# Optimization experiments

Measured on AMD Instinct MI355X. Metric: run time of the kernel, lower is better.

## Reference

```python
import jax, jax.numpy as jnp
import numpy as np

STATE_BITS = 10          # L: bits of trellis state
SHIFT_BITS = 2           # K: bits shifted in per step -> 2^K predecessors
CHUNK = 4                # chunk_size: values emitted per trellis step
S = 1 << STATE_BITS      # number of states (codebook rows)
NPRED = 1 << SHIFT_BITS  # predecessors per state
HI = 1 << (STATE_BITS - SHIFT_BITS)


def setup_inputs() -> dict:
    key = jax.random.key(0)
    k1, k2 = jax.random.split(key)
    array = jax.random.normal(k1, (1024, 1024), dtype=jnp.float32)
    codebook = jax.random.normal(k2, (S, CHUNK), dtype=jnp.float32)
    return {"array": array, "codebook": codebook, "block_size": 16}


def _viterbi(x, codebook):
    # x: [T, CHUNK, B] target chunks; codebook: [S, CHUNK]
    # Exact min-squared-error Viterbi over the bit-shift trellis:
    #   next_state = ((prev << K) | new_bits) mod 2^L
    # Predecessors of state s: (s >> K) + j * 2^(L-K), j in [0, 2^K)
    s = jnp.arange(S)
    prev_idx = (s[:, None] >> SHIFT_BITS) + jnp.arange(NPRED)[None, :] * HI  # [S, NPRED]
    cnorm = jnp.sum(codebook * codebook, axis=1)  # [S]

    def cost(xt):  # xt: [CHUNK, B] -> [S, B] squared distances
        return cnorm[:, None] - 2.0 * (codebook @ xt) + jnp.sum(xt * xt, axis=0)[None, :]

    alpha0 = cost(x[0])  # free initial state: cost of emitting first chunk

    def step(alpha, xt):
        cand = alpha[prev_idx]                        # [S, NPRED, B]
        j = jnp.argmin(cand, axis=1)                  # [S, B]
        alpha_new = jnp.min(cand, axis=1) + cost(xt)  # [S, B]
        return alpha_new, j.astype(jnp.int8)

    alpha_T, bps = jax.lax.scan(step, alpha0, x[1:])  # bps: [T-1, S, B] int8
    last = jnp.argmin(alpha_T, axis=0).astype(jnp.int32)  # [B] state at step T-1

    def back(state, bp):
        # state: [B] state at step t; bp: [S, B] backpointers into step t
        j = jnp.take_along_axis(bp, state[None, :], axis=0)[0].astype(jnp.int32)
        prev = (state >> SHIFT_BITS) + j * HI
        return prev, state

    first, rest = jax.lax.scan(back, last, bps, reverse=True)
    return jnp.concatenate([first[None], rest], axis=0)  # [T, B] int32


def reference(array, codebook, block_size):
    rows, columns = array.shape
    br, bc = rows // block_size, columns // block_size
    epb = block_size * block_size          # elements_per_block
    T = epb // CHUNK                       # number_of_steps
    B = br * bc                            # number_of_blocks
    # block reshape: [rows, cols] -> [elements_per_block, number_of_blocks]
    blocks = (array.reshape(br, block_size, bc, block_size)
                   .transpose(0, 2, 1, 3)
                   .reshape(B, epb).T)
    x = blocks.reshape(T, CHUNK, B)
    states = _viterbi(x, codebook)         # [T, B]
    vals = codebook[states]                # [T, B, CHUNK] gather reconstruct
    rec = vals.transpose(0, 2, 1).reshape(epb, B)
    rec = (rec.T.reshape(br, bc, block_size, block_size)
              .transpose(0, 2, 1, 3)
              .reshape(rows, columns))
    states_out = states.T.reshape(br, bc, T)
    return rec, states_out
```

## Files before the change

### kernel.cpp

```cpp
#include <hip/hip_runtime.h>


#define COLS      1024
#define T_STEPS   64
#define REC_SIZE  (1024 * 1024)

__global__ __launch_bounds__(256)
__attribute__((amdgpu_waves_per_eu(4, 8)))
void viterbi_q(
    const float* __restrict__ arr,
    const float* __restrict__ cbook,
    float* __restrict__ out)
{
    const int tid   = threadIdx.x;
    const int lane  = tid & 63;
    const int wid   = tid >> 6;
    const int chain = blockIdx.x;
    const int rb    = chain >> 6;
    const int cb    = chain & 63;

    __shared__ __align__(16) float tile[256];
    __shared__ __align__(16) float Mbuf[2][256];
    __shared__ unsigned char J[63 * 256];
    __shared__ int   st_lds[64];
    __shared__ float redv[4];
    __shared__ int   reds[4];

    if (tid < 64) {
        const int r  = tid >> 2;
        const int c4 = (tid & 3) << 2;
        float4 v = *(const float4*)(arr + (rb * 16 + r) * COLS + cb * 16 + c4);
        *(float4*)&tile[tid << 2] = v;
    }
    Mbuf[0][tid] = 0.f;

    float4 a[4];
    float  h[4];
    #pragma unroll
    for (int j = 0; j < 4; ++j) {
        float4 v = *(const float4*)(cbook + (tid + (j << 8)) * 4);
        a[j] = v;
        h[j] = -0.5f * (v.x * v.x + v.y * v.y + v.z * v.z + v.w * v.w);
    }

    __syncthreads();

#define STEP(T, RB, WB)                                                       \
    {                                                                         \
        const float4 xt = *(const float4*)&tile[(T) << 2];                    \
        float cand[4];                                                        \
        _Pragma("unroll")                                                     \
        for (int j = 0; j < 4; ++j) {                                         \
            const float m = Mbuf[RB][(tid >> 2) + (j << 6)];                  \
            float acc = fmaf(a[j].x, xt.x, h[j]);                             \
            acc = fmaf(a[j].y, xt.y, acc);                                    \
            acc = fmaf(a[j].z, xt.z, acc);                                    \
            acc = fmaf(a[j].w, xt.w, acc);                                    \
            cand[j] = acc + m;                                                \
        }                                                                     \
        const float v = fmaxf(fmaxf(fmaxf(cand[0], cand[1]), cand[2]),        \
                              cand[3]);                                       \
        const int jidx = (cand[0] == v) ? 0                                   \
                       : (cand[1] == v) ? 1                                   \
                       : (cand[2] == v) ? 2 : 3;                              \
        Mbuf[WB][tid] = v;                                                    \
        J[(T) * 256 + tid] = (unsigned char)jidx;                             \
    }

    #pragma unroll 1
    for (int t = 0; t < 62; t += 2) {
        STEP(t, 0, 1);
        __syncthreads();
        STEP(t + 1, 1, 0);
        __syncthreads();
    }
    STEP(62, 0, 1);
    __syncthreads();
#undef STEP

    {
        const float4 xt = *(const float4*)&tile[63 << 2];
        float bv = -3.4e38f;
        int   bs = 0;
        #pragma unroll
        for (int j = 0; j < 4; ++j) {
            const float m = Mbuf[1][(tid >> 2) + (j << 6)];
            float acc = fmaf(a[j].x, xt.x, h[j]);
            acc = fmaf(a[j].y, xt.y, acc);
            acc = fmaf(a[j].z, xt.z, acc);
            acc = fmaf(a[j].w, xt.w, acc);
            acc += m;
            if (acc > bv) { bv = acc; bs = tid + (j << 8); }
        }
        #pragma unroll
        for (int off = 32; off > 0; off >>= 1) {
            const float ov = __shfl_xor(bv, off, 64);
            const int   os = __shfl_xor(bs, off, 64);
            if (ov > bv || (ov == bv && os < bs)) { bv = ov; bs = os; }
        }
        if (lane == 0) { redv[wid] = bv; reds[wid] = bs; }
    }
    __syncthreads();

    if (tid == 0) {
        float gv = redv[0];
        int   gs = reds[0];
        #pragma unroll
        for (int w = 1; w < 4; ++w) {
            if (redv[w] > gv || (redv[w] == gv && reds[w] < gs)) {
                gv = redv[w];
                gs = reds[w];
            }
        }
        int s = gs;
        st_lds[T_STEPS - 1] = s;
        for (int i = T_STEPS - 2; i >= 0; --i) {
            const int p = s >> 2;
            const int j = J[i * 256 + p];
            s = p + (j << 8);
            st_lds[i] = s;
        }
    }
    __syncthreads();

    if (tid < 64) {
        const int st = st_lds[tid];
        out[REC_SIZE + chain * 64 + tid] = (float)st;
        const float4 v = *(const float4*)(cbook + st * 4);
        const int r  = tid >> 2;
        const int c4 = (tid & 3) << 2;
        *(float4*)(out + (rb * 16 + r) * COLS + cb * 16 + c4) = v;
    }
}

extern "C" void kernel_launch(void* const* d_in, const int* in_sizes, int n_in,
                              void* d_out, int out_size, void* d_ws, size_t ws_size,
                              hipStream_t stream)
{
    const float* arr   = (const float*)d_in[0];
    const float* cbook = (const float*)d_in[1];
    float* out = (float*)d_out;
    viterbi_q<<<dim3(4096), dim3(256), 0, stream>>>(arr, cbook, out);
}
```

Before: 110.1 us.

## Process two trellis chains per block and pack backpointers with ballots

Each 256-thread block now runs two independent Viterbi chains, so one barrier per step serves both and the codebook registers are shared across them. The backpointers are stored as ballot bitmasks (two 64-bit words per wave per step) instead of one byte per state, which shrinks LDS use and the per-step stores. The grid is halved and waves_per_eu is raised to a minimum of 8. The extra work per step adds register pressure, and the serial traceback now walks two chains at once.

```diff
diff --git a/kernel.cpp b/kernel.cpp
--- a/kernel.cpp
+++ b/kernel.cpp
@@ -6,33 +6,35 @@
 #define REC_SIZE  (1024 * 1024)
 
 __global__ __launch_bounds__(256)
-__attribute__((amdgpu_waves_per_eu(4, 8)))
+__attribute__((amdgpu_waves_per_eu(8, 8)))
 void viterbi_q(
     const float* __restrict__ arr,
     const float* __restrict__ cbook,
     float* __restrict__ out)
 {
-    const int tid   = threadIdx.x;
-    const int lane  = tid & 63;
-    const int wid   = tid >> 6;
-    const int chain = blockIdx.x;
-    const int rb    = chain >> 6;
-    const int cb    = chain & 63;
+    const int tid  = threadIdx.x;
+    const int lane = tid & 63;
+    const int wid  = tid >> 6;
 
-    __shared__ __align__(16) float tile[256];
-    __shared__ __align__(16) float Mbuf[2][256];
-    __shared__ unsigned char J[63 * 256];
-    __shared__ int   st_lds[64];
-    __shared__ float redv[4];
-    __shared__ int   reds[4];
+    __shared__ __align__(16) float tile[2][256];
+    __shared__ __align__(16) float Mb[2][2][256];
+    __shared__ __align__(16) ulonglong2 J64[2][63 * 4];
+    __shared__ int   st_lds[2][64];
+    __shared__ float redv[2][4];
+    __shared__ int   reds[2][4];
 
-    if (tid < 64) {
-        const int r  = tid >> 2;
-        const int c4 = (tid & 3) << 2;
+    if (tid < 128) {
+        const int ch    = tid >> 6;
+        const int e     = tid & 63;
+        const int chain = (blockIdx.x << 1) | ch;
+        const int rb    = chain >> 6, cb = chain & 63;
+        const int r  = e >> 2;
+        const int c4 = (e & 3) << 2;
         float4 v = *(const float4*)(arr + (rb * 16 + r) * COLS + cb * 16 + c4);
-        *(float4*)&tile[tid << 2] = v;
+        *(float4*)&tile[ch][e << 2] = v;
     }
-    Mbuf[0][tid] = 0.f;
+    Mb[0][0][tid] = 0.f;
+    Mb[1][0][tid] = 0.f;
 
     float4 a[4];
     float  h[4];
@@ -45,90 +47,138 @@
 
     __syncthreads();
 
-#define STEP(T, RB, WB)                                                       \
+#define STEP2(T, RB, WB)                                                      \
     {                                                                         \
-        const float4 xt = *(const float4*)&tile[(T) << 2];                    \
-        float cand[4];                                                        \
+        const float4 xtA = *(const float4*)&tile[0][(T) << 2];                \
+        const float4 xtB = *(const float4*)&tile[1][(T) << 2];                \
+        float mjA[4], mjB[4];                                                 \
+        _Pragma("unroll")                                                     \
+        for (int j = 0; j < 4; ++j) mjA[j] = Mb[0][RB][(tid >> 2) + (j << 6)];\
+        _Pragma("unroll")                                                     \
+        for (int j = 0; j < 4; ++j) mjB[j] = Mb[1][RB][(tid >> 2) + (j << 6)];\
+        float candA[4], candB[4];                                             \
         _Pragma("unroll")                                                     \
         for (int j = 0; j < 4; ++j) {                                         \
-            const float m = Mbuf[RB][(tid >> 2) + (j << 6)];                  \
-            float acc = fmaf(a[j].x, xt.x, h[j]);                             \
-            acc = fmaf(a[j].y, xt.y, acc);                                    \
-            acc = fmaf(a[j].z, xt.z, acc);                                    \
-            acc = fmaf(a[j].w, xt.w, acc);                                    \
-            cand[j] = acc + m;                                                \
+            float acc = fmaf(a[j].x, xtA.x, h[j]);                            \
+            acc = fmaf(a[j].y, xtA.y, acc);                                   \
+            acc = fmaf(a[j].z, xtA.z, acc);                                   \
+            acc = fmaf(a[j].w, xtA.w, acc);                                   \
+            candA[j] = acc + mjA[j];                                          \
         }                                                                     \
-        const float v = fmaxf(fmaxf(fmaxf(cand[0], cand[1]), cand[2]),        \
-                              cand[3]);                                       \
-        const int jidx = (cand[0] == v) ? 0                                   \
-                       : (cand[1] == v) ? 1                                   \
-                       : (cand[2] == v) ? 2 : 3;                              \
-        Mbuf[WB][tid] = v;                                                    \
-        J[(T) * 256 + tid] = (unsigned char)jidx;                             \
+        _Pragma("unroll")                                                     \
+        for (int j = 0; j < 4; ++j) {                                         \
+            float acc = fmaf(a[j].x, xtB.x, h[j]);                            \
+            acc = fmaf(a[j].y, xtB.y, acc);                                   \
+            acc = fmaf(a[j].z, xtB.z, acc);                                   \
+            acc = fmaf(a[j].w, xtB.w, acc);                                   \
+            candB[j] = acc + mjB[j];                                          \
+        }                                                                     \
+        const float vA = fmaxf(fmaxf(fmaxf(candA[0], candA[1]), candA[2]),    \
+                               candA[3]);                                     \
+        const int jA = (candA[0] == vA) ? 0                                   \
+                     : (candA[1] == vA) ? 1                                   \
+                     : (candA[2] == vA) ? 2 : 3;                              \
+        const float vB = fmaxf(fmaxf(fmaxf(candB[0], candB[1]), candB[2]),    \
+                               candB[3]);                                     \
+        const int jB = (candB[0] == vB) ? 0                                   \
+                     : (candB[1] == vB) ? 1                                   \
+                     : (candB[2] == vB) ? 2 : 3;                              \
+        Mb[0][WB][tid] = vA;                                                  \
+        Mb[1][WB][tid] = vB;                                                  \
+        const unsigned long long a0 = __ballot(jA & 1);                       \
+        const unsigned long long a1 = __ballot(jA & 2);                       \
+        const unsigned long long b0 = __ballot(jB & 1);                       \
+        const unsigned long long b1 = __ballot(jB & 2);                       \
+        if (lane == 0) {                                                      \
+            ulonglong2 pa; pa.x = a0; pa.y = a1;                              \
+            ulonglong2 pb; pb.x = b0; pb.y = b1;                              \
+            J64[0][((T) << 2) | wid] = pa;                                    \
+            J64[1][((T) << 2) | wid] = pb;                                    \
+        }                                                                     \
+        __syncthreads();                                                      \
     }
 
     #pragma unroll 1
     for (int t = 0; t < 62; t += 2) {
-        STEP(t, 0, 1);
-        __syncthreads();
-        STEP(t + 1, 1, 0);
-        __syncthreads();
+        STEP2(t, 0, 1)
+        STEP2(t + 1, 1, 0)
     }
-    STEP(62, 0, 1);
-    __syncthreads();
-#undef STEP
+    STEP2(62, 0, 1)
+#undef STEP2
 
     {
-        const float4 xt = *(const float4*)&tile[63 << 2];
-        float bv = -3.4e38f;
-        int   bs = 0;
+        const float4 xtA = *(const float4*)&tile[0][63 << 2];
+        const float4 xtB = *(const float4*)&tile[1][63 << 2];
+        float bvA = -3.4e38f, bvB = -3.4e38f;
+        int   bsA = 0,        bsB = 0;
         #pragma unroll
         for (int j = 0; j < 4; ++j) {
-            const float m = Mbuf[1][(tid >> 2) + (j << 6)];
-            float acc = fmaf(a[j].x, xt.x, h[j]);
-            acc = fmaf(a[j].y, xt.y, acc);
-            acc = fmaf(a[j].z, xt.z, acc);
-            acc = fmaf(a[j].w, xt.w, acc);
-            acc += m;
-            if (acc > bv) { bv = acc; bs = tid + (j << 8); }
+            const float mA = Mb[0][1][(tid >> 2) + (j << 6)];
+            const float mB = Mb[1][1][(tid >> 2) + (j << 6)];
+            float accA = fmaf(a[j].x, xtA.x, h[j]);
+            accA = fmaf(a[j].y, xtA.y, accA);
+            accA = fmaf(a[j].z, xtA.z, accA);
+            accA = fmaf(a[j].w, xtA.w, accA);
+            accA += mA;
+            if (accA > bvA) { bvA = accA; bsA = tid + (j << 8); }
+            float accB = fmaf(a[j].x, xtB.x, h[j]);
+            accB = fmaf(a[j].y, xtB.y, accB);
+            accB = fmaf(a[j].z, xtB.z, accB);
+            accB = fmaf(a[j].w, xtB.w, accB);
+            accB += mB;
+            if (accB > bvB) { bvB = accB; bsB = tid + (j << 8); }
         }
         #pragma unroll
         for (int off = 32; off > 0; off >>= 1) {
-            const float ov = __shfl_xor(bv, off, 64);
-            const int   os = __shfl_xor(bs, off, 64);
-            if (ov > bv || (ov == bv && os < bs)) { bv = ov; bs = os; }
+            const float ovA = __shfl_xor(bvA, off, 64);
+            const int   osA = __shfl_xor(bsA, off, 64);
+            const float ovB = __shfl_xor(bvB, off, 64);
+            const int   osB = __shfl_xor(bsB, off, 64);
+            if (ovA > bvA || (ovA == bvA && osA < bsA)) { bvA = ovA; bsA = osA; }
+            if (ovB > bvB || (ovB == bvB && osB < bsB)) { bvB = ovB; bsB = osB; }
         }
-        if (lane == 0) { redv[wid] = bv; reds[wid] = bs; }
-    }
-    __syncthreads();
-
-    if (tid == 0) {
-        float gv = redv[0];
-        int   gs = reds[0];
-        #pragma unroll
-        for (int w = 1; w < 4; ++w) {
-            if (redv[w] > gv || (redv[w] == gv && reds[w] < gs)) {
-                gv = redv[w];
-                gs = reds[w];
-            }
-        }
-        int s = gs;
-        st_lds[T_STEPS - 1] = s;
-        for (int i = T_STEPS - 2; i >= 0; --i) {
-            const int p = s >> 2;
-            const int j = J[i * 256 + p];
-            s = p + (j << 8);
-            st_lds[i] = s;
+        if (lane == 0) {
+            redv[0][wid] = bvA; reds[0][wid] = bsA;
+            redv[1][wid] = bvB; reds[1][wid] = bsB;
         }
     }
     __syncthreads();
 
-    if (tid < 64) {
-        const int st = st_lds[tid];
-        out[REC_SIZE + chain * 64 + tid] = (float)st;
+    if (tid < 2) {
+        const int ch = tid;
+        float gv = redv[ch][0];
+        int   gs = reds[ch][0];
+        #pragma unroll
+        for (int w = 1; w < 4; ++w) {
+            if (redv[ch][w] > gv || (redv[ch][w] == gv && reds[ch][w] < gs)) {
+                gv = redv[ch][w];
+                gs = reds[ch][w];
+            }
+        }
+        int s = gs;
+        st_lds[ch][T_STEPS - 1] = s;
+        for (int i = T_STEPS - 2; i >= 0; --i) {
+            const int p = s >> 2;
+            const ulonglong2 bb = J64[ch][(i << 2) | (p >> 6)];
+            const int l = p & 63;
+            const int j = (int)((bb.x >> l) & 1ull) |
+                          ((int)((bb.y >> l) & 1ull) << 1);
+            s = p + (j << 8);
+            st_lds[ch][i] = s;
+        }
+    }
+    __syncthreads();
+
+    if (tid < 128) {
+        const int ch = tid >> 6;
+        const int t  = tid & 63;
+        const int chain = (blockIdx.x << 1) | ch;
+        const int rb = chain >> 6, cb = chain & 63;
+        const int st = st_lds[ch][t];
+        out[REC_SIZE + chain * 64 + t] = (float)st;
         const float4 v = *(const float4*)(cbook + st * 4);
-        const int r  = tid >> 2;
-        const int c4 = (tid & 3) << 2;
+        const int r  = t >> 2;
+        const int c4 = (t & 3) << 2;
         *(float4*)(out + (rb * 16 + r) * COLS + cb * 16 + c4) = v;
     }
 }
@@ -140,5 +190,5 @@
     const float* arr   = (const float*)d_in[0];
     const float* cbook = (const float*)d_in[1];
     float* out = (float*)d_out;
-    viterbi_q<<<dim3(4096), dim3(256), 0, stream>>>(arr, cbook, out);
+    viterbi_q<<<dim3(2048), dim3(256), 0, stream>>>(arr, cbook, out);
 }
```

Result: slower. 124.8 us (+13.4%).
